# Optimization experiments

Measured on AMD Instinct MI355X. Metric: run time of the kernel, lower is better.

## Reference

```python
import jax, jax.numpy as jnp
import numpy as np

B, S, F, E, H, L = 16, 256, 512, 128, 64, 8


def _gru(x, Wih, Whh, bih, bhh):
    """torch-style GRU over time. x: [B,S,E] -> hidden states [B,S,H]."""
    xp = jnp.einsum('bse,ge->bsg', x, Wih) + bih  # [B,S,3H]

    def step(h, xt):
        gh = h @ Whh.T + bhh                      # [B,3H]
        xr, xz, xn = jnp.split(xt, 3, axis=-1)
        hr, hz, hn = jnp.split(gh, 3, axis=-1)
        r = jax.nn.sigmoid(xr + hr)
        z = jax.nn.sigmoid(xz + hz)
        n = jnp.tanh(xn + r * hn)
        h_new = (1.0 - z) * n + z * h
        return h_new, h_new

    h0 = jnp.zeros((x.shape[0], Whh.shape[1]), x.dtype)
    _, hs = jax.lax.scan(step, h0, jnp.swapaxes(xp, 0, 1))  # [S,B,H]
    return jnp.swapaxes(hs, 0, 1)


def setup_inputs() -> dict:
    ks = jax.random.split(jax.random.key(0), 24)
    u = lambda k, shape, n: jax.random.uniform(k, shape, jnp.float32, -1.0 / np.sqrt(n), 1.0 / np.sqrt(n))
    inp = {
        'X': jax.random.normal(ks[0], (B, S, F), jnp.float32),
        'M': jnp.ones((B, S), jnp.float32),
        'cur_M': jax.random.uniform(ks[1], (B, S), jnp.float32),
        # embed linear [E,F]
        'W_embed': u(ks[2], (E, F), F), 'b_embed': u(ks[3], (E,), F),
        # GRU alpha
        'Wih_a': u(ks[4], (3 * H, E), H), 'Whh_a': u(ks[5], (3 * H, H), H),
        'bih_a': u(ks[6], (3 * H,), H), 'bhh_a': u(ks[7], (3 * H,), H),
        # GRU beta
        'Wih_b': u(ks[8], (3 * H, E), H), 'Whh_b': u(ks[9], (3 * H, H), H),
        'bih_b': u(ks[10], (3 * H,), H), 'bhh_b': u(ks[11], (3 * H,), H),
        # attention linears
        'Wb': u(ks[12], (E, H), H), 'bb': u(ks[13], (E,), H),
        'Wa': u(ks[14], (1, H), H), 'ba': u(ks[15], (1,), H),
        # predict linear
        'Wp': u(ks[16], (L, E), E), 'bp': u(ks[17], (L,), E),
    }
    return inp


def reference(X, M, cur_M, W_embed, b_embed,
              Wih_a, Whh_a, bih_a, bhh_a,
              Wih_b, Whh_b, bih_b, bhh_b,
              Wb, bb, Wa, ba, Wp, bp):
    n_seq = X.shape[1]
    emb = jnp.einsum('bsf,ef->bse', X, W_embed) + b_embed          # [B,S,E]
    h_alpha = _gru(emb, Wih_a, Whh_a, bih_a, bhh_a)                # [B,S,H]
    h_beta = _gru(emb, Wih_b, Whh_b, bih_b, bhh_b)                 # [B,S,H]

    # RETAIN attention
    beta_w = jnp.tanh(jnp.einsum('bsh,eh->bse', h_beta, Wb) + bb)  # [B,S,E]
    corr = (jnp.einsum('bsh,oh->bso', h_alpha, Wa) + ba)[..., 0]   # [B,S]
    attn = jnp.exp(corr)                                           # [B,S] (indexed by j)
    flag = jnp.triu(jnp.ones((n_seq, n_seq), X.dtype))             # flag[i,j]=1 iff j>=i
    flag_m = flag[None, :, :] * M[:, None, :]                      # [B,S,S]
    num = attn[:, None, :] * flag_m                                # [B,i,j]
    denom = num.sum(-1, keepdims=True) + 1e-10                     # [B,S,1]
    alpha_w = num / denom                                          # [B,S,S]
    # sum_j alpha[b,i,j] * beta_w[b,j,:] * emb[b,j,:]  (same math as the
    # original broadcasted [B,S,S,E] product, without materializing it)
    weighted = jnp.einsum('bij,bje->bie', alpha_w, beta_w * emb)   # [B,S,E]

    all_output = (jnp.einsum('bse,le->bsl', weighted, Wp) + bp) * M[..., None]  # [B,S,L]
    cur_output = (all_output * cur_M[..., None]).sum(axis=1)                    # [B,L]
    return all_output, cur_output
```

## Files before the change

kernel.cpp:

```cpp
#include <hip/hip_runtime.h>
#include <math.h>

#define BB 16
#define SS 256
#define FF 512
#define EE 128
#define HH 64
#define GG 192
#define LL 8

__device__ __forceinline__ float sigmoid_f(float x) {
    return 1.0f / (1.0f + __expf(-x));
}
__device__ __forceinline__ float tanh_f(float x) {
    return 1.0f - 2.0f / (1.0f + __expf(2.0f * x));
}

__device__ __forceinline__ void gemm_bt_body(
    const float* __restrict__ A, const float* __restrict__ Bm,
    const float* __restrict__ bias, float* __restrict__ C,
    int N, int K)
{
    __shared__ float As[32][68];
    __shared__ float Bs[64][68];
    const int t = threadIdx.x;
    const int row0 = blockIdx.x * 32;
    const int col0 = blockIdx.y * 64;
    const int tr = t & 7;
    const int tc = t >> 3;
    float acc[4][2] = {{0.f,0.f},{0.f,0.f},{0.f,0.f},{0.f,0.f}};

    for (int k0 = 0; k0 < K; k0 += 64) {
        {
            int r = t >> 3;
            int q = t & 7;
            const float* src = &A[(size_t)(row0 + r) * K + k0];
            #pragma unroll
            for (int it = 0; it < 2; ++it) {
                int kk = (q + it * 8) * 4;
                *(float4*)&As[r][kk] = *(const float4*)&src[kk];
            }
        }
        {
            int r = t >> 2;
            int q = t & 3;
            int n = col0 + r;
            #pragma unroll
            for (int it = 0; it < 4; ++it) {
                int kk = (q + it * 4) * 4;
                float4 v = {0.f, 0.f, 0.f, 0.f};
                if (n < N) v = *(const float4*)&Bm[(size_t)n * K + k0 + kk];
                *(float4*)&Bs[r][kk] = v;
            }
        }
        __syncthreads();
        #pragma unroll
        for (int k = 0; k < 64; k += 4) {
            float4 av[4], bv[2];
            #pragma unroll
            for (int i = 0; i < 4; ++i) av[i] = *(const float4*)&As[tr + 8*i][k];
            #pragma unroll
            for (int j = 0; j < 2; ++j) bv[j] = *(const float4*)&Bs[tc + 32*j][k];
            #pragma unroll
            for (int i = 0; i < 4; ++i)
                #pragma unroll
                for (int j = 0; j < 2; ++j)
                    acc[i][j] += av[i].x*bv[j].x + av[i].y*bv[j].y
                               + av[i].z*bv[j].z + av[i].w*bv[j].w;
        }
        __syncthreads();
    }

    #pragma unroll
    for (int i = 0; i < 4; ++i) {
        int r = row0 + tr + 8*i;
        #pragma unroll
        for (int j = 0; j < 2; ++j) {
            int c = col0 + tc + 32*j;
            if (c < N) C[(size_t)r * N + c] = acc[i][j] + bias[c];
        }
    }
}

__global__ __launch_bounds__(256) void gemm_bt(
    const float* __restrict__ A, const float* __restrict__ Bm,
    const float* __restrict__ bias, float* __restrict__ C,
    int N, int K)
{
    gemm_bt_body(A, Bm, bias, C, N, K);
}

__global__ __launch_bounds__(256) void gemm_bt_dual(
    const float* __restrict__ A,
    const float* __restrict__ B0, const float* __restrict__ bias0, float* __restrict__ C0,
    const float* __restrict__ B1, const float* __restrict__ bias1, float* __restrict__ C1,
    int N, int K)
{
    const float* Bm   = blockIdx.z ? B1    : B0;
    const float* bias = blockIdx.z ? bias1 : bias0;
    float*       C    = blockIdx.z ? C1    : C0;
    gemm_bt_body(A, Bm, bias, C, N, K);
}

__global__ __launch_bounds__(192, 1)
__attribute__((amdgpu_waves_per_eu(1, 1)))
void gru_kernel(
    const float* __restrict__ xpa, const float* __restrict__ xpb,
    const float* __restrict__ Whh_a, const float* __restrict__ bhh_a,
    const float* __restrict__ Whh_b, const float* __restrict__ bhh_b,
    float* __restrict__ hs_a, float* __restrict__ hs_b)
{
    const int blk = blockIdx.x;
    const int b = blk >> 1;
    const int which = blk & 1;
    const float* xp  = which ? xpb   : xpa;
    const float* Whh = which ? Whh_b : Whh_a;
    const float* bhh = which ? bhh_b : bhh_a;
    float* hs        = which ? hs_b  : hs_a;

    const int t = threadIdx.x;
    const int g = t >> 6;
    const int j = t & 63;

    __shared__ float gh_s[2][GG];

    float4 w[16];
    {
        const float4* wrow = (const float4*)&Whh[(size_t)(g * 64 + j) * HH];
        #pragma unroll
        for (int k = 0; k < 16; ++k) {
            w[k] = wrow[k];
            asm volatile("" : "+v"(w[k].x), "+v"(w[k].y), "+v"(w[k].z), "+v"(w[k].w));
        }
    }
    const float bh = bhh[g * 64 + j];

    const float* xrow = xp + (size_t)b * SS * GG;
    float* hrow = hs + (size_t)b * SS * HH;
    float hcur = 0.f;

    float xg = xrow[g * 64 + j];
    float xn = xrow[128 + j];

#define RL(v, k) __int_as_float(__builtin_amdgcn_readlane(__float_as_int(v), (k)))

    for (int s = 0; s < SS; ++s) {
        const float* nx = xrow + GG;
        float nxg = nx[g * 64 + j];
        float nxn = nx[128 + j];

        float a0 = bh, a1 = 0.f, a2 = 0.f, a3 = 0.f;
        #pragma unroll
        for (int k = 0; k < 16; ++k) {
            float4 wk = w[k];
            float h0 = RL(hcur, 4*k + 0);
            float h1 = RL(hcur, 4*k + 1);
            float h2 = RL(hcur, 4*k + 2);
            float h3 = RL(hcur, 4*k + 3);
            a0 = fmaf(wk.x, h0, a0);
            a1 = fmaf(wk.y, h1, a1);
            a2 = fmaf(wk.z, h2, a2);
            a3 = fmaf(wk.w, h3, a3);
        }
        float pre = (a0 + a1) + (a2 + a3);
        gh_s[s & 1][t] = (g < 2) ? (xg + pre) : pre;

        asm volatile("s_waitcnt lgkmcnt(0)" ::: "memory");
        __builtin_amdgcn_s_barrier();
        asm volatile("" ::: "memory");

        float ghr = gh_s[s & 1][j];
        float ghz = gh_s[s & 1][64 + j];
        float ghn = gh_s[s & 1][128 + j];
        float r = sigmoid_f(ghr);
        float z = sigmoid_f(ghz);
        float n = tanh_f(xn + r * ghn);
        hcur = fmaf(z, hcur - n, n);
        if (g == 0) hrow[j] = hcur;

        xg = nxg; xn = nxn;
        xrow += GG;
        hrow += HH;
    }
#undef RL
}

__global__ __launch_bounds__(128) void attn_val_kernel(
    const float* __restrict__ h_alpha, const float* __restrict__ h_beta,
    const float* __restrict__ emb, const float* __restrict__ M,
    const float* __restrict__ Wa, const float* __restrict__ ba,
    const float* __restrict__ Wb, const float* __restrict__ bb,
    float* __restrict__ val, float* __restrict__ wj)
{
    const int bj = blockIdx.x;
    const int t = threadIdx.x;
    __shared__ float hb_s[HH];
    __shared__ float wj_s;

    if (t < 64) {
        hb_s[t] = h_beta[(size_t)bj * HH + t];
        float p = h_alpha[(size_t)bj * HH + t] * Wa[t];
        #pragma unroll
        for (int off = 32; off > 0; off >>= 1) p += __shfl_down(p, off);
        if (t == 0) {
            float a = __expf(p + ba[0]) * M[bj];
            wj_s = a;
            wj[bj] = a;
        }
    }
    __syncthreads();

    float acc = bb[t];
    const float4* wrow = (const float4*)&Wb[(size_t)t * HH];
    #pragma unroll
    for (int k = 0; k < 16; ++k) {
        float4 w4 = wrow[k];
        float4 h4 = *(const float4*)&hb_s[k * 4];
        acc += w4.x*h4.x + w4.y*h4.y + w4.z*h4.z + w4.w*h4.w;
    }
    float bw = tanh_f(acc);
    val[(size_t)bj * EE + t] = bw * emb[(size_t)bj * EE + t] * wj_s;
}

__global__ __launch_bounds__(128) void scan_kernel(
    const float* __restrict__ val, const float* __restrict__ wj,
    float* __restrict__ wtd)
{
    const int b = blockIdx.x;
    const int t = threadIdx.x;
    float se = 0.f;
    float d = 1e-10f;
    for (int j = SS - 1; j >= 0; --j) {
        size_t idx = ((size_t)(b * SS + j)) * EE + t;
        se += val[idx];
        d += wj[b * SS + j];
        wtd[idx] = se / d;
    }
}

__global__ __launch_bounds__(256) void proj_kernel(
    const float* __restrict__ wtd, const float* __restrict__ Wp,
    const float* __restrict__ bp, const float* __restrict__ M,
    float* __restrict__ out)
{
    __shared__ float wt_s[32][132];
    __shared__ float wp_s[8][132];
    const int t = threadIdx.x;
    const int row0 = blockIdx.x * 32;

    {
        int r = t >> 3;
        int q = t & 7;
        const float* src = &wtd[(size_t)(row0 + r) * EE];
        #pragma unroll
        for (int it = 0; it < 4; ++it) {
            int kk = (q + it * 8) * 4;
            *(float4*)&wt_s[r][kk] = *(const float4*)&src[kk];
        }
    }
    {
        int r = t >> 5;
        int q = t & 31;
        *(float4*)&wp_s[r][q * 4] = *(const float4*)&Wp[(size_t)r * EE + q * 4];
    }
    __syncthreads();

    const int r = t >> 3, l = t & 7;
    float acc = 0.f;
    #pragma unroll
    for (int i = 0; i < 32; ++i) {
        float4 a = *(const float4*)&wt_s[r][i * 4];
        float4 w = *(const float4*)&wp_s[l][i * 4];
        acc += a.x*w.x + a.y*w.y + a.z*w.z + a.w*w.w;
    }
    const int row = row0 + r;
    out[(size_t)row * LL + l] = (acc + bp[l]) * M[row];
}

__global__ __launch_bounds__(256) void cur_kernel(
    const float* __restrict__ out_all, const float* __restrict__ curM,
    float* __restrict__ out_cur)
{
    const int b = blockIdx.x;
    const int t = threadIdx.x;
    const int l = t & 7, c = t >> 3;
    float p = 0.f;
    #pragma unroll
    for (int k = 0; k < 8; ++k) {
        int s = c + k * 32;
        p += out_all[((size_t)(b * SS + s)) * LL + l] * curM[b * SS + s];
    }
    __shared__ float red[32][9];
    red[c][l] = p;
    __syncthreads();
    if (t < 8) {
        float sum = 0.f;
        for (int c2 = 0; c2 < 32; ++c2) sum += red[c2][t];
        out_cur[b * LL + t] = sum;
    }
}

extern "C" void kernel_launch(void* const* d_in, const int* in_sizes, int n_in,
                              void* d_out, int out_size, void* d_ws, size_t ws_size,
                              hipStream_t stream)
{
    const float* X       = (const float*)d_in[0];
    const float* M       = (const float*)d_in[1];
    const float* cur_M   = (const float*)d_in[2];
    const float* W_embed = (const float*)d_in[3];
    const float* b_embed = (const float*)d_in[4];
    const float* Wih_a   = (const float*)d_in[5];
    const float* Whh_a   = (const float*)d_in[6];
    const float* bih_a   = (const float*)d_in[7];
    const float* bhh_a   = (const float*)d_in[8];
    const float* Wih_b   = (const float*)d_in[9];
    const float* Whh_b   = (const float*)d_in[10];
    const float* bih_b   = (const float*)d_in[11];
    const float* bhh_b   = (const float*)d_in[12];
    const float* Wb      = (const float*)d_in[13];
    const float* bb      = (const float*)d_in[14];
    const float* Wa      = (const float*)d_in[15];
    const float* ba      = (const float*)d_in[16];
    const float* Wp      = (const float*)d_in[17];
    const float* bp      = (const float*)d_in[18];
    float* out = (float*)d_out;

    float* ws  = (float*)d_ws;
    float* emb = ws;
    float* xpa = emb + (size_t)BB*SS*EE;
    float* xpb = xpa + (size_t)BB*SS*GG;
    float* ha  = xpb + (size_t)BB*SS*GG;
    float* hb  = ha  + (size_t)BB*SS*HH;
    float* val = hb  + (size_t)BB*SS*HH;
    float* wjv = val + (size_t)BB*SS*EE;
    float* wtd = wjv + (size_t)BB*SS;

    const int ROWS = BB * SS;

    gemm_bt<<<dim3(ROWS/32, EE/64), 256, 0, stream>>>(X, W_embed, b_embed, emb, EE, FF);
    gemm_bt_dual<<<dim3(ROWS/32, (GG+63)/64, 2), 256, 0, stream>>>(
        emb, Wih_a, bih_a, xpa, Wih_b, bih_b, xpb, GG, EE);
    gru_kernel<<<32, 192, 0, stream>>>(xpa, xpb, Whh_a, bhh_a, Whh_b, bhh_b, ha, hb);
    attn_val_kernel<<<ROWS, 128, 0, stream>>>(ha, hb, emb, M, Wa, ba, Wb, bb, val, wjv);
    scan_kernel<<<BB, 128, 0, stream>>>(val, wjv, wtd);
    proj_kernel<<<ROWS/32, 256, 0, stream>>>(wtd, Wp, bp, M, out);
    cur_kernel<<<BB, 256, 0, stream>>>(out, cur_M, out + (size_t)BB*SS*LL);
}
```

Before: 203.5 us.

## Split GRU recurrent dot product across two waves per gate (K-split)

The GRU recurrence kernel now launches 384 threads instead of 192. Each gate row's 64-element dot product with the hidden state is split into two halves handled by separate waves, and the partial sums are combined through shared memory after the barrier. This halves the serial readlane/FMA chain per step, which sits on the latency-critical sequential path. In exchange, every thread does extra LDS reads and adds, and six waves now have to synchronise at each barrier instead of three.

```diff
diff --git a/kernel.cpp b/kernel.cpp
--- a/kernel.cpp
+++ b/kernel.cpp
@@ -102,8 +102,7 @@
     gemm_bt_body(A, Bm, bias, C, N, K);
 }
 
-__global__ __launch_bounds__(192, 1)
-__attribute__((amdgpu_waves_per_eu(1, 1)))
+__global__ __launch_bounds__(384)
 void gru_kernel(
     const float* __restrict__ xpa, const float* __restrict__ xpb,
     const float* __restrict__ Whh_a, const float* __restrict__ bhh_a,
@@ -119,21 +118,23 @@
     float* hs        = which ? hs_b  : hs_a;
 
     const int t = threadIdx.x;
-    const int g = t >> 6;
+    const int w = t >> 6;
+    const int g = w >> 1;
+    const int hf = w & 1;
     const int j = t & 63;
 
-    __shared__ float gh_s[2][GG];
-
-    float4 w[16];
+    __shared__ float p_s[2][6][64];
+
+    float4 wv[8];
     {
-        const float4* wrow = (const float4*)&Whh[(size_t)(g * 64 + j) * HH];
-        #pragma unroll
-        for (int k = 0; k < 16; ++k) {
-            w[k] = wrow[k];
-            asm volatile("" : "+v"(w[k].x), "+v"(w[k].y), "+v"(w[k].z), "+v"(w[k].w));
-        }
-    }
-    const float bh = bhh[g * 64 + j];
+        const float4* wrow = (const float4*)&Whh[(size_t)(g * 64 + j) * HH + hf * 32];
+        #pragma unroll
+        for (int k = 0; k < 8; ++k) {
+            wv[k] = wrow[k];
+            asm volatile("" : "+v"(wv[k].x), "+v"(wv[k].y), "+v"(wv[k].z), "+v"(wv[k].w));
+        }
+    }
+    const float bh = (hf == 0) ? bhh[g * 64 + j] : 0.f;
 
     const float* xrow = xp + (size_t)b * SS * GG;
     float* hrow = hs + (size_t)b * SS * HH;
@@ -151,32 +152,30 @@
 
         float a0 = bh, a1 = 0.f, a2 = 0.f, a3 = 0.f;
         #pragma unroll
-        for (int k = 0; k < 16; ++k) {
-            float4 wk = w[k];
-            float h0 = RL(hcur, 4*k + 0);
-            float h1 = RL(hcur, 4*k + 1);
-            float h2 = RL(hcur, 4*k + 2);
-            float h3 = RL(hcur, 4*k + 3);
-            a0 = fmaf(wk.x, h0, a0);
-            a1 = fmaf(wk.y, h1, a1);
-            a2 = fmaf(wk.z, h2, a2);
-            a3 = fmaf(wk.w, h3, a3);
-        }
-        float pre = (a0 + a1) + (a2 + a3);
-        gh_s[s & 1][t] = (g < 2) ? (xg + pre) : pre;
+        for (int k = 0; k < 8; ++k) {
+            float4 wk = wv[k];
+            const int kb = hf * 32 + 4 * k;
+            a0 = fmaf(wk.x, RL(hcur, kb + 0), a0);
+            a1 = fmaf(wk.y, RL(hcur, kb + 1), a1);
+            a2 = fmaf(wk.z, RL(hcur, kb + 2), a2);
+            a3 = fmaf(wk.w, RL(hcur, kb + 3), a3);
+        }
+        float part = (a0 + a1) + (a2 + a3);
+        if (g < 2 && hf == 0) part += xg;
+        p_s[s & 1][w][j] = part;
 
         asm volatile("s_waitcnt lgkmcnt(0)" ::: "memory");
         __builtin_amdgcn_s_barrier();
         asm volatile("" ::: "memory");
 
-        float ghr = gh_s[s & 1][j];
-        float ghz = gh_s[s & 1][64 + j];
-        float ghn = gh_s[s & 1][128 + j];
-        float r = sigmoid_f(ghr);
-        float z = sigmoid_f(ghz);
-        float n = tanh_f(xn + r * ghn);
+        float pr = p_s[s & 1][0][j] + p_s[s & 1][1][j];
+        float pz = p_s[s & 1][2][j] + p_s[s & 1][3][j];
+        float pn = p_s[s & 1][4][j] + p_s[s & 1][5][j];
+        float r = sigmoid_f(pr);
+        float z = sigmoid_f(pz);
+        float n = tanh_f(xn + r * pn);
         hcur = fmaf(z, hcur - n, n);
-        if (g == 0) hrow[j] = hcur;
+        if (w == 0) hrow[j] = hcur;
 
         xg = nxg; xn = nxn;
         xrow += GG;
@@ -340,7 +339,7 @@
     gemm_bt<<<dim3(ROWS/32, EE/64), 256, 0, stream>>>(X, W_embed, b_embed, emb, EE, FF);
     gemm_bt_dual<<<dim3(ROWS/32, (GG+63)/64, 2), 256, 0, stream>>>(
         emb, Wih_a, bih_a, xpa, Wih_b, bih_b, xpb, GG, EE);
-    gru_kernel<<<32, 192, 0, stream>>>(xpa, xpb, Whh_a, bhh_a, Whh_b, bhh_b, ha, hb);
+    gru_kernel<<<32, 384, 0, stream>>>(xpa, xpb, Whh_a, bhh_a, Whh_b, bhh_b, ha, hb);
     attn_val_kernel<<<ROWS, 128, 0, stream>>>(ha, hb, emb, M, Wa, ba, Wb, bb, val, wjv);
     scan_kernel<<<BB, 128, 0, stream>>>(val, wjv, wtd);
     proj_kernel<<<ROWS/32, 256, 0, stream>>>(wtd, Wp, bp, M, out);
```

Measured after the change: 300.8 us. 1.48x slower.

## Parallelize reverse suffix scan into tiled two-pass scan across more blocks

Applied to the files above, without the earlier changes.

The reverse cumulative sum that produced the attention-weighted output ran with one block per batch and a serial 256-step loop. It is now split into a tile-sum pass and a tile-local scan pass seeded with the suffix of the tile totals, giving 16x more blocks. The cost is one extra launch, extra workspace, and re-reading val. The GRU weight load is also changed to volatile element-wise loads, likely to alter code generation or register placement.

```diff
diff --git a/kernel.cpp b/kernel.cpp
--- a/kernel.cpp
+++ b/kernel.cpp
@@ -8,6 +8,7 @@
 #define HH 64
 #define GG 192
 #define LL 8
+#define TT 16
 
 __device__ __forceinline__ float sigmoid_f(float x) {
     return 1.0f / (1.0f + __expf(-x));
@@ -126,11 +127,14 @@
 
     float4 w[16];
     {
-        const float4* wrow = (const float4*)&Whh[(size_t)(g * 64 + j) * HH];
+        const volatile float4* wrow =
+            (const volatile float4*)&Whh[(size_t)(g * 64 + j) * HH];
         #pragma unroll
         for (int k = 0; k < 16; ++k) {
-            w[k] = wrow[k];
-            asm volatile("" : "+v"(w[k].x), "+v"(w[k].y), "+v"(w[k].z), "+v"(w[k].w));
+            float4 v;
+            v.x = wrow[k].x; v.y = wrow[k].y; v.z = wrow[k].z; v.w = wrow[k].w;
+            asm volatile("" : "+v"(v.x), "+v"(v.y), "+v"(v.z), "+v"(v.w));
+            w[k] = v;
         }
     }
     const float bh = bhh[g * 64 + j];
@@ -222,18 +226,47 @@
     val[(size_t)bj * EE + t] = bw * emb[(size_t)bj * EE + t] * wj_s;
 }
 
-__global__ __launch_bounds__(128) void scan_kernel(
+__global__ __launch_bounds__(128) void scanA_kernel(
     const float* __restrict__ val, const float* __restrict__ wj,
+    float* __restrict__ tsum, float* __restrict__ wsum)
+{
+    const int b = blockIdx.x, tt = blockIdx.y;
+    const int e = threadIdx.x;
+    const int j0 = tt * 16;
+    float s = 0.f;
+    #pragma unroll
+    for (int jj = 0; jj < 16; ++jj)
+        s += val[((size_t)(b * SS + j0 + jj)) * EE + e];
+    tsum[((size_t)(b * TT + tt)) * EE + e] = s;
+
+    if (e < 16) {
+        float p = wj[b * SS + j0 + e];
+        #pragma unroll
+        for (int off = 8; off > 0; off >>= 1) p += __shfl_down(p, off, 16);
+        if (e == 0) wsum[b * TT + tt] = p;
+    }
+}
+
+__global__ __launch_bounds__(128) void scanB_kernel(
+    const float* __restrict__ val, const float* __restrict__ wj,
+    const float* __restrict__ tsum, const float* __restrict__ wsum,
     float* __restrict__ wtd)
 {
-    const int b = blockIdx.x;
-    const int t = threadIdx.x;
+    const int b = blockIdx.x, tt = blockIdx.y;
+    const int e = threadIdx.x;
+    const int j0 = tt * 16;
+
     float se = 0.f;
+    for (int t2 = tt + 1; t2 < TT; ++t2)
+        se += tsum[((size_t)(b * TT + t2)) * EE + e];
     float d = 1e-10f;
-    for (int j = SS - 1; j >= 0; --j) {
-        size_t idx = ((size_t)(b * SS + j)) * EE + t;
+    for (int t2 = tt + 1; t2 < TT; ++t2)
+        d += wsum[b * TT + t2];
+
+    for (int jj = 15; jj >= 0; --jj) {
+        size_t idx = ((size_t)(b * SS + j0 + jj)) * EE + e;
         se += val[idx];
-        d += wj[b * SS + j];
+        d += wj[b * SS + j0 + jj];
         wtd[idx] = se / d;
     }
 }
@@ -334,6 +367,8 @@
     float* val = hb  + (size_t)BB*SS*HH;
     float* wjv = val + (size_t)BB*SS*EE;
     float* wtd = wjv + (size_t)BB*SS;
+    float* tsum = wtd + (size_t)BB*SS*EE;
+    float* wsum = tsum + (size_t)BB*TT*EE;
 
     const int ROWS = BB * SS;
 
@@ -342,7 +377,8 @@
         emb, Wih_a, bih_a, xpa, Wih_b, bih_b, xpb, GG, EE);
     gru_kernel<<<32, 192, 0, stream>>>(xpa, xpb, Whh_a, bhh_a, Whh_b, bhh_b, ha, hb);
     attn_val_kernel<<<ROWS, 128, 0, stream>>>(ha, hb, emb, M, Wa, ba, Wb, bb, val, wjv);
-    scan_kernel<<<BB, 128, 0, stream>>>(val, wjv, wtd);
+    scanA_kernel<<<dim3(BB, TT), 128, 0, stream>>>(val, wjv, tsum, wsum);
+    scanB_kernel<<<dim3(BB, TT), 128, 0, stream>>>(val, wjv, tsum, wsum, wtd);
     proj_kernel<<<ROWS/32, 256, 0, stream>>>(wtd, Wp, bp, M, out);
     cur_kernel<<<BB, 256, 0, stream>>>(out, cur_M, out + (size_t)BB*SS*LL);
 }
```

After: 188.6 us. 7.3% less time.
